# Performance work log

Hardware: AMD Instinct MI355X
Metric: run time of the kernel (lower is better)

Reference implementation:

```python
import jax, jax.numpy as jnp
import numpy as np

B, S, E, H, V, T, L = 64, 512, 512, 512, 32000, 2, 1


def setup_inputs() -> dict:
    key = jax.random.key(0)
    ks = jax.random.split(key, 12)
    # xavier_normal std for h0/c0 of shape (L, B, H): fan_in=B*H, fan_out=L*H
    xav = float(np.sqrt(2.0 / (B * H + L * H)))
    s = 1.0 / float(np.sqrt(H))  # pytorch LSTM default uniform bound
    return {
        "sentence": jax.random.randint(ks[0], (B, S), 0, V, dtype=jnp.int64),
        "h0": jax.random.normal(ks[1], (L, B, H), jnp.float32) * xav,
        "c0": jax.random.normal(ks[2], (L, B, H), jnp.float32) * xav,
        "emb": jax.random.normal(ks[3], (V, E), jnp.float32),
        "W_ih": jax.random.uniform(ks[4], (4 * H, E), jnp.float32, -s, s),
        "W_hh": jax.random.uniform(ks[5], (4 * H, H), jnp.float32, -s, s),
        "b_ih": jax.random.uniform(ks[6], (4 * H,), jnp.float32, -s, s),
        "b_hh": jax.random.uniform(ks[7], (4 * H,), jnp.float32, -s, s),
        "W_lin": jax.random.uniform(ks[8], (T, H), jnp.float32, -s, s),
        "b_lin": jax.random.uniform(ks[9], (T,), jnp.float32, -s, s),
    }


def reference(sentence, h0, c0, emb, W_ih, W_hh, b_ih, b_hh, W_lin, b_lin):
    x = emb[sentence]                                   # [B,S,E]
    # precompute input-to-gate projections for all timesteps
    xg = jnp.einsum("bse,ge->bsg", x, W_ih) + (b_ih + b_hh)  # [B,S,4H]

    def step(carry, xt):
        h, c = carry                                    # [B,H] each
        g = xt + h @ W_hh.T                             # [B,4H]
        i, f, gc, o = jnp.split(g, 4, axis=-1)          # torch gate order i,f,g,o
        i = jax.nn.sigmoid(i)
        f = jax.nn.sigmoid(f)
        gc = jnp.tanh(gc)
        o = jax.nn.sigmoid(o)
        c = f * c + i * gc
        h = o * jnp.tanh(c)
        return (h, c), h

    (hn, cn), hs = jax.lax.scan(step, (h0[0], c0[0]), xg.transpose(1, 0, 2))
    lstm_out = hs.transpose(1, 0, 2)                    # [B,S,H]
    # dropout is identity at inference; torch code indexes drop[-1,:,:] =
    # LAST BATCH SAMPLE (batch_first=True quirk) -> [S,H]
    last = lstm_out[-1]                                 # [S,H]
    return last @ W_lin.T + b_lin                       # [S,T]
```

## Files before the change

kernel.cpp:

```cpp
#include <hip/hip_runtime.h>
#include <hip/hip_bf16.h>


#define NB 64

#define HIDX(e) ((((e) >> 4) * 20) + ((e) & 15))

__global__ __launch_bounds__(256) void xg_gemm_k(
    const int* __restrict__ sent, const float* __restrict__ emb,
    const float* __restrict__ W_ih, const float* __restrict__ b_ih,
    const float* __restrict__ b_hh, float* __restrict__ xg)
{
    __shared__ float As[16][65];
    __shared__ float Bs[16][65];
    __shared__ int aidx[64];
    const int tid = threadIdx.x;
    const int t0 = blockIdx.x * 64;
    const int n0 = blockIdx.y * 64;
    if (tid < 64) aidx[tid] = sent[63 * 512 + t0 + tid];
    __syncthreads();

    const int kk = tid & 15;
    const int mm = tid >> 4;
    const int tx = tid & 15, ty = tid >> 4;
    float acc[4][4] = {};

    for (int kb = 0; kb < 512; kb += 16) {
        #pragma unroll
        for (int j = 0; j < 4; j++) {
            int m = mm + j * 16;
            As[kk][m] = emb[(size_t)aidx[m] * 512 + kb + kk];
            Bs[kk][m] = W_ih[(size_t)(n0 + m) * 512 + kb + kk];
        }
        __syncthreads();
        #pragma unroll
        for (int k = 0; k < 16; k++) {
            float a[4], bv[4];
            #pragma unroll
            for (int i = 0; i < 4; i++) a[i] = As[k][ty * 4 + i];
            #pragma unroll
            for (int j = 0; j < 4; j++) bv[j] = Bs[k][tx * 4 + j];
            #pragma unroll
            for (int i = 0; i < 4; i++)
                #pragma unroll
                for (int j = 0; j < 4; j++)
                    acc[i][j] += a[i] * bv[j];
        }
        __syncthreads();
    }

    #pragma unroll
    for (int i = 0; i < 4; i++) {
        int t = t0 + ty * 4 + i;
        #pragma unroll
        for (int j = 0; j < 4; j++) {
            int col = n0 + tx * 4 + j;
            xg[(size_t)t * 2048 + col] = acc[i][j] + b_ih[col] + b_hh[col];
        }
    }
}

__global__ __launch_bounds__(256, 1) void lstm_seq_k(
    const float* __restrict__ h0, const float* __restrict__ c0,
    const float* __restrict__ W_hh, const float* __restrict__ xg,
    float* __restrict__ hs,
    unsigned long long* __restrict__ sA,
    unsigned long long* __restrict__ sB)
{
    __shared__ float hbuf[32 * 20];
    __shared__ float gacc[32];
    __shared__ float cbuf[8];

    const int tid = threadIdx.x;
    const int b = blockIdx.x;
    const int cg = tid & 31;
    const int rg = tid >> 5;

    int grow[4];
    #pragma unroll
    for (int r = 0; r < 4; r++) {
        int rl = rg * 4 + r;
        grow[r] = (rl >> 3) * 512 + b * 8 + (rl & 7);
    }

    float4 wv[4][4];
    #pragma unroll
    for (int r = 0; r < 4; r++)
        #pragma unroll
        for (int cq = 0; cq < 4; cq++)
            wv[r][cq] = *(const float4*)&W_hh[(size_t)grow[r] * 512 + cg * 16 + cq * 4];

    if (tid < 8) cbuf[tid] = c0[63 * 512 + b * 8 + tid];
    __syncthreads();

    for (int t = 0; t < 512; t++) {
        float xgp[4];
        if (cg == 0) {
            #pragma unroll
            for (int r = 0; r < 4; r++)
                xgp[r] = xg[(size_t)t * 2048 + grow[r]];
        }

        if (t == 0) {
            hbuf[HIDX(tid)]       = h0[63 * 512 + tid];
            hbuf[HIDX(tid + 256)] = h0[63 * 512 + tid + 256];
        } else {
            unsigned long long* src = ((t - 1) & 1) ? sB : sA;
            unsigned long long* p0 = &src[tid];
            unsigned long long* p1 = &src[tid + 256];
            const unsigned int expt = (unsigned int)t;
            unsigned long long v0, v1;
            for (;;) {
                v0 = __hip_atomic_load(p0, __ATOMIC_RELAXED, __HIP_MEMORY_SCOPE_AGENT);
                v1 = __hip_atomic_load(p1, __ATOMIC_RELAXED, __HIP_MEMORY_SCOPE_AGENT);
                if ((unsigned int)(v0 >> 32) == expt &&
                    (unsigned int)(v1 >> 32) == expt) break;
            }
            hbuf[HIDX(tid)]       = __uint_as_float((unsigned int)v0);
            hbuf[HIDX(tid + 256)] = __uint_as_float((unsigned int)v1);
        }
        __syncthreads();

        float4 hv[4];
        #pragma unroll
        for (int cq = 0; cq < 4; cq++)
            hv[cq] = *(const float4*)&hbuf[cg * 20 + cq * 4];

        float acc[4];
        #pragma unroll
        for (int r = 0; r < 4; r++) {
            float s = 0.f;
            #pragma unroll
            for (int cq = 0; cq < 4; cq++) {
                s += wv[r][cq].x * hv[cq].x;
                s += wv[r][cq].y * hv[cq].y;
                s += wv[r][cq].z * hv[cq].z;
                s += wv[r][cq].w * hv[cq].w;
            }
            acc[r] = s;
        }

        #pragma unroll
        for (int r = 0; r < 4; r++) {
            #pragma unroll
            for (int m = 16; m >= 1; m >>= 1)
                acc[r] += __shfl_xor(acc[r], m, 64);
        }
        if (cg == 0) {
            #pragma unroll
            for (int r = 0; r < 4; r++)
                gacc[rg * 4 + r] = acc[r] + xgp[r];
        }
        __syncthreads();

        if (tid < 8) {
            float gi = gacc[tid];
            float gf = gacc[8 + tid];
            float gc = gacc[16 + tid];
            float go = gacc[24 + tid];
            float ii = 1.f / (1.f + __expf(-gi));
            float ff = 1.f / (1.f + __expf(-gf));
            float cc = 1.f - 2.f / (__expf(2.f * gc) + 1.f);
            float oo = 1.f / (1.f + __expf(-go));
            float cn = ff * cbuf[tid] + ii * cc;
            cbuf[tid] = cn;
            float th = 1.f - 2.f / (__expf(2.f * cn) + 1.f);
            float hval = oo * th;

            hs[(size_t)t * 512 + b * 8 + tid] = hval;

            unsigned long long* dst = (t & 1) ? sB : sA;
            unsigned long long pv =
                ((unsigned long long)(unsigned int)(t + 1) << 32) |
                (unsigned long long)__float_as_uint(hval);
            __hip_atomic_store(&dst[b * 8 + tid], pv,
                               __ATOMIC_RELAXED, __HIP_MEMORY_SCOPE_AGENT);
        }
    }
}

__global__ __launch_bounds__(256) void final_linear_k(
    const float* __restrict__ hs, const float* __restrict__ W_lin,
    const float* __restrict__ b_lin, float* __restrict__ out)
{
    const int tid = threadIdx.x;
    const int wave = tid >> 6;
    const int lane = tid & 63;
    const int s = blockIdx.x * 4 + wave;
    const float* h = hs + (size_t)s * 512;
    float a0 = 0.f, a1 = 0.f;
    #pragma unroll
    for (int k0 = 0; k0 < 512; k0 += 64) {
        float hv = h[k0 + lane];
        a0 += hv * W_lin[k0 + lane];
        a1 += hv * W_lin[512 + k0 + lane];
    }
    #pragma unroll
    for (int m = 32; m >= 1; m >>= 1) {
        a0 += __shfl_xor(a0, m, 64);
        a1 += __shfl_xor(a1, m, 64);
    }
    if (lane == 0) {
        out[s * 2]     = a0 + b_lin[0];
        out[s * 2 + 1] = a1 + b_lin[1];
    }
}

extern "C" void kernel_launch(void* const* d_in, const int* in_sizes, int n_in,
                              void* d_out, int out_size, void* d_ws, size_t ws_size,
                              hipStream_t stream)
{
    const int*   sent  = (const int*)d_in[0];
    const float* h0    = (const float*)d_in[1];
    const float* c0    = (const float*)d_in[2];
    const float* emb   = (const float*)d_in[3];
    const float* W_ih  = (const float*)d_in[4];
    const float* W_hh  = (const float*)d_in[5];
    const float* b_ih  = (const float*)d_in[6];
    const float* b_hh  = (const float*)d_in[7];
    const float* W_lin = (const float*)d_in[8];
    const float* b_lin = (const float*)d_in[9];
    float* out = (float*)d_out;

    char* ws = (char*)d_ws;
    float* xg = (float*)ws;
    float* hs = (float*)(ws + 4 * 1024 * 1024);
    unsigned long long* sA = (unsigned long long*)(ws + 5 * 1024 * 1024);
    unsigned long long* sB = (unsigned long long*)(ws + 5 * 1024 * 1024 + 4096);

    hipMemsetAsync(sA, 0, 2 * 4096, stream);

    dim3 g1(8, 32);
    xg_gemm_k<<<g1, 256, 0, stream>>>(sent, emb, W_ih, b_ih, b_hh, xg);
    lstm_seq_k<<<NB, 256, 0, stream>>>(h0, c0, W_hh, xg, hs, sA, sB);
    final_linear_k<<<128, 256, 0, stream>>>(hs, W_lin, b_lin, out);
}
```

Before: 984.3 us.

## Regroup LSTM gate rows per hidden unit and fuse gate math per half-wave

Each 32-lane group now owns one hidden unit and computes all four of its gates (i,f,g,o). That lets the gate nonlinearity and cell update run in registers right after the shuffle reduction, which removes the gacc shared buffer and one __syncthreads per timestep. W_hh is moved from registers into a 64KB shared-memory array in a permuted layout. The xg output is also permuted so the four gate values for a hidden unit sit next to each other. In exchange, every timestep now reads the weights from shared memory instead of registers, which adds LDS traffic and latency on the serial critical path.

After: 1.214 ms. 23.4% more time.

```diff
diff --git a/kernel.cpp b/kernel.cpp
--- a/kernel.cpp
+++ b/kernel.cpp
@@ -55,7 +55,9 @@
         #pragma unroll
         for (int j = 0; j < 4; j++) {
             int col = n0 + tx * 4 + j;
-            xg[(size_t)t * 2048 + col] = acc[i][j] + b_ih[col] + b_hh[col];
+            int q = col >> 9, bb = (col >> 3) & 63, jj = col & 7;
+            xg[(size_t)t * 2048 + bb * 32 + q * 8 + jj] =
+                acc[i][j] + b_ih[col] + b_hh[col];
         }
     }
 }
@@ -67,52 +69,53 @@
     unsigned long long* __restrict__ sA,
     unsigned long long* __restrict__ sB)
 {
+    __shared__ float lw[32 * 512];
     __shared__ float hbuf[32 * 20];
-    __shared__ float gacc[32];
-    __shared__ float cbuf[8];
 
     const int tid = threadIdx.x;
     const int b = blockIdx.x;
     const int cg = tid & 31;
     const int rg = tid >> 5;
-
-    int grow[4];
-    #pragma unroll
-    for (int r = 0; r < 4; r++) {
-        int rl = rg * 4 + r;
-        grow[r] = (rl >> 3) * 512 + b * 8 + (rl & 7);
-    }
-
-    float4 wv[4][4];
-    #pragma unroll
-    for (int r = 0; r < 4; r++)
-        #pragma unroll
-        for (int cq = 0; cq < 4; cq++)
-            wv[r][cq] = *(const float4*)&W_hh[(size_t)grow[r] * 512 + cg * 16 + cq * 4];
-
-    if (tid < 8) cbuf[tid] = c0[63 * 512 + b * 8 + tid];
+    const int hidx = b * 8 + rg;
+
+    {
+        const int lr  = tid >> 3;
+        const int seg = tid & 7;
+        const int q   = lr >> 3;
+        const int jj  = lr & 7;
+        const float* src = &W_hh[(size_t)(q * 512 + b * 8 + jj) * 512 + seg * 64];
+        #pragma unroll
+        for (int f = 0; f < 16; f++) {
+            float4 v = *(const float4*)&src[f * 4];
+            int c0i = seg * 64 + f * 4;
+            float vv[4] = {v.x, v.y, v.z, v.w};
+            #pragma unroll
+            for (int e4 = 0; e4 < 4; e4++) {
+                int c = c0i + e4;
+                lw[(lr * 8 + ((c & 15) >> 1)) * 64 + (c >> 4) * 2 + (c & 1)] = vv[e4];
+            }
+        }
+    }
+
+    float creg = c0[63 * 512 + hidx];
     __syncthreads();
 
     for (int t = 0; t < 512; t++) {
         float xgp[4];
-        if (cg == 0) {
-            #pragma unroll
-            for (int r = 0; r < 4; r++)
-                xgp[r] = xg[(size_t)t * 2048 + grow[r]];
-        }
+        #pragma unroll
+        for (int q = 0; q < 4; q++)
+            xgp[q] = xg[(size_t)t * 2048 + b * 32 + q * 8 + rg];
 
         if (t == 0) {
             hbuf[HIDX(tid)]       = h0[63 * 512 + tid];
             hbuf[HIDX(tid + 256)] = h0[63 * 512 + tid + 256];
         } else {
             unsigned long long* src = ((t - 1) & 1) ? sB : sA;
-            unsigned long long* p0 = &src[tid];
-            unsigned long long* p1 = &src[tid + 256];
             const unsigned int expt = (unsigned int)t;
             unsigned long long v0, v1;
             for (;;) {
-                v0 = __hip_atomic_load(p0, __ATOMIC_RELAXED, __HIP_MEMORY_SCOPE_AGENT);
-                v1 = __hip_atomic_load(p1, __ATOMIC_RELAXED, __HIP_MEMORY_SCOPE_AGENT);
+                v0 = __hip_atomic_load(&src[tid],       __ATOMIC_RELAXED, __HIP_MEMORY_SCOPE_AGENT);
+                v1 = __hip_atomic_load(&src[tid + 256], __ATOMIC_RELAXED, __HIP_MEMORY_SCOPE_AGENT);
                 if ((unsigned int)(v0 >> 32) == expt &&
                     (unsigned int)(v1 >> 32) == expt) break;
             }
@@ -121,59 +124,54 @@
         }
         __syncthreads();
 
-        float4 hv[4];
-        #pragma unroll
-        for (int cq = 0; cq < 4; cq++)
-            hv[cq] = *(const float4*)&hbuf[cg * 20 + cq * 4];
+        float hvf[16];
+        #pragma unroll
+        for (int i4 = 0; i4 < 4; i4++) {
+            float4 v = *(const float4*)&hbuf[cg * 20 + i4 * 4];
+            hvf[i4 * 4 + 0] = v.x; hvf[i4 * 4 + 1] = v.y;
+            hvf[i4 * 4 + 2] = v.z; hvf[i4 * 4 + 3] = v.w;
+        }
 
         float acc[4];
         #pragma unroll
-        for (int r = 0; r < 4; r++) {
+        for (int q = 0; q < 4; q++) {
+            const float* wrow = &lw[((q * 8 + rg) * 8) * 64 + cg * 2];
             float s = 0.f;
             #pragma unroll
-            for (int cq = 0; cq < 4; cq++) {
-                s += wv[r][cq].x * hv[cq].x;
-                s += wv[r][cq].y * hv[cq].y;
-                s += wv[r][cq].z * hv[cq].z;
-                s += wv[r][cq].w * hv[cq].w;
+            for (int kp = 0; kp < 8; kp++) {
+                float2 wv = *(const float2*)&wrow[kp * 64];
+                s += wv.x * hvf[kp * 2 + 0];
+                s += wv.y * hvf[kp * 2 + 1];
             }
-            acc[r] = s;
-        }
-
-        #pragma unroll
-        for (int r = 0; r < 4; r++) {
+            acc[q] = s;
+        }
+
+        #pragma unroll
+        for (int q = 0; q < 4; q++) {
             #pragma unroll
             for (int m = 16; m >= 1; m >>= 1)
-                acc[r] += __shfl_xor(acc[r], m, 64);
-        }
+                acc[q] += __shfl_xor(acc[q], m, 64);
+        }
+
+        float gi = acc[0] + xgp[0];
+        float gf = acc[1] + xgp[1];
+        float gg = acc[2] + xgp[2];
+        float go = acc[3] + xgp[3];
+        float ii = 1.f / (1.f + __expf(-gi));
+        float ff = 1.f / (1.f + __expf(-gf));
+        float cc = 1.f - 2.f / (__expf(2.f * gg) + 1.f);
+        float oo = 1.f / (1.f + __expf(-go));
+        creg = ff * creg + ii * cc;
+        float th = 1.f - 2.f / (__expf(2.f * creg) + 1.f);
+        float hval = oo * th;
+
         if (cg == 0) {
-            #pragma unroll
-            for (int r = 0; r < 4; r++)
-                gacc[rg * 4 + r] = acc[r] + xgp[r];
-        }
-        __syncthreads();
-
-        if (tid < 8) {
-            float gi = gacc[tid];
-            float gf = gacc[8 + tid];
-            float gc = gacc[16 + tid];
-            float go = gacc[24 + tid];
-            float ii = 1.f / (1.f + __expf(-gi));
-            float ff = 1.f / (1.f + __expf(-gf));
-            float cc = 1.f - 2.f / (__expf(2.f * gc) + 1.f);
-            float oo = 1.f / (1.f + __expf(-go));
-            float cn = ff * cbuf[tid] + ii * cc;
-            cbuf[tid] = cn;
-            float th = 1.f - 2.f / (__expf(2.f * cn) + 1.f);
-            float hval = oo * th;
-
-            hs[(size_t)t * 512 + b * 8 + tid] = hval;
-
+            hs[(size_t)t * 512 + hidx] = hval;
             unsigned long long* dst = (t & 1) ? sB : sA;
             unsigned long long pv =
                 ((unsigned long long)(unsigned int)(t + 1) << 32) |
                 (unsigned long long)__float_as_uint(hval);
-            __hip_atomic_store(&dst[b * 8 + tid], pv,
+            __hip_atomic_store(&dst[hidx], pv,
                                __ATOMIC_RELAXED, __HIP_MEMORY_SCOPE_AGENT);
         }
     }
```
